# Optimization experiments

Measured on AMD Instinct MI355X. Metric: run time of the kernel, lower is better.

The kernel has to match this reference:

```python
import jax, jax.numpy as jnp
import numpy as np

B, L, S, D, H = 4, 2048, 2048, 1024, 16
HD = D // H


def setup_inputs() -> dict:
    key = jax.random.key(0)
    ks = jax.random.split(key, 7)
    scale = 1.0 / np.sqrt(D)
    q = jax.random.normal(ks[0], (B, L, D), dtype=jnp.float32)
    k = jax.random.normal(ks[1], (B, S, D), dtype=jnp.float32)
    v = jax.random.normal(ks[2], (B, S, D), dtype=jnp.float32)
    # causal mask, broadcast over batch and heads; 0 -> masked
    mask = jnp.tril(jnp.ones((L, S), dtype=jnp.int32))[None, None]
    Wq = jax.random.normal(ks[3], (D, D), dtype=jnp.float32) * scale
    Wk = jax.random.normal(ks[4], (D, D), dtype=jnp.float32) * scale
    Wv = jax.random.normal(ks[5], (D, D), dtype=jnp.float32) * scale
    Wo = jax.random.normal(ks[6], (D, D), dtype=jnp.float32) * scale
    return {"q": q, "k": k, "v": v, "mask": mask,
            "Wq": Wq, "Wk": Wk, "Wv": Wv, "Wo": Wo}


def reference(q, k, v, mask, Wq, Wk, Wv, Wo):
    Bq, Lq, _ = q.shape
    Sk = k.shape[1]
    # torch nn.Linear: y = x @ W.T  (W is [out, in])
    qh = (q @ Wq.T).reshape(Bq, Lq, H, HD).transpose(0, 2, 1, 3)  # [B,H,L,hd]
    kh = (k @ Wk.T).reshape(Bq, Sk, H, HD).transpose(0, 2, 1, 3)  # [B,H,S,hd]
    vh = (v @ Wv.T).reshape(Bq, Sk, H, HD).transpose(0, 2, 1, 3)  # [B,H,S,hd]
    scores = jnp.einsum('bhld,bhsd->bhls', qh, kh) / jnp.sqrt(jnp.float32(HD))
    scores = jnp.where(mask == 0, -jnp.inf, scores)
    attn = jax.nn.softmax(scores, axis=-1)
    out = jnp.einsum('bhls,bhsd->bhld', attn, vh)
    out = out.transpose(0, 2, 1, 3).reshape(Bq, Lq, D)
    return out @ Wo.T
```

## Files before the change

### kernel.cpp

```cpp
#include <hip/hip_runtime.h>
#include <hip/hip_bf16.h>

#define BB 4
#define LL 2048
#define SS 2048
#define DD 1024
#define HH 16
#define HD 64

typedef __bf16 bf16;
typedef __attribute__((ext_vector_type(8))) __bf16 bf16x8;
typedef __attribute__((ext_vector_type(4))) float f32x4;

#define ASYNC16(gp, lp)                                                        \
  __builtin_amdgcn_global_load_lds(                                            \
      (__attribute__((address_space(1))) void*)(gp),                           \
      (__attribute__((address_space(3))) void*)(lp), 16, 0, 0)

__global__ __launch_bounds__(256) void detect_dtype(
    const unsigned short* __restrict__ qbits, int* __restrict__ flag) {
  __shared__ int smax;
  if (threadIdx.x == 0) smax = 0;
  __syncthreads();
  int m = 0;
  for (int i = threadIdx.x; i < 4096; i += 256) {
    const int e = (qbits[i] >> 7) & 0xFF;
    m = m > e ? m : e;
  }
  atomicMax(&smax, m);
  __syncthreads();
  if (threadIdx.x == 0) *flag = (smax >= 0xC0) ? 1 : 0;
}

__global__ __launch_bounds__(256) void convert_all(
    const void* __restrict__ q, const void* __restrict__ k,
    const void* __restrict__ v, const void* __restrict__ Wq,
    const void* __restrict__ Wk, const void* __restrict__ Wv,
    const void* __restrict__ Wo, bf16* __restrict__ cq, bf16* __restrict__ ck,
    bf16* __restrict__ cv, bf16* __restrict__ cWq, bf16* __restrict__ cWk,
    bf16* __restrict__ cWv, bf16* __restrict__ cWo,
    const int* __restrict__ flag) {
  const int b = blockIdx.x;
  const void* src;
  bf16* dst;
  int lb;
  if (b < 12288) {
    const int t = b >> 12;
    lb = b & 4095;
    src = (t == 0) ? q : (t == 1) ? k : v;
    dst = (t == 0) ? cq : (t == 1) ? ck : cv;
  } else {
    const int t = (b - 12288) >> 9;
    lb = (b - 12288) & 511;
    src = (t == 0) ? Wq : (t == 1) ? Wk : (t == 2) ? Wv : Wo;
    dst = (t == 0) ? cWq : (t == 1) ? cWk : (t == 2) ? cWv : cWo;
  }
  const int i8 = (lb * 256 + threadIdx.x) * 8;
  if (*flag) {
    const float4* s = (const float4*)src;
    const float4 a = s[i8 / 4];
    const float4 c = s[i8 / 4 + 1];
    bf16x8 o;
    o[0] = (bf16)a.x; o[1] = (bf16)a.y; o[2] = (bf16)a.z; o[3] = (bf16)a.w;
    o[4] = (bf16)c.x; o[5] = (bf16)c.y; o[6] = (bf16)c.z; o[7] = (bf16)c.w;
    *(bf16x8*)(dst + i8) = o;
  } else {
    *(uint4*)(dst + i8) = ((const uint4*)src)[i8 / 8];
  }
}

#define GM 8192
#define GN 1024
#define GK 1024

#define GEMM_BODY(X, W)                                                        \
  const int tid = threadIdx.x;                                                 \
  const int lane = tid & 63;                                                   \
  const int wave = tid >> 6;                                                   \
  const int l15 = lane & 15;                                                   \
  const int quad = lane >> 4;                                                  \
  const int wm = wave >> 1;                                                    \
  const int wn = wave & 1;                                                     \
  const int lin = blockIdx.y * 8 + blockIdx.x;                                 \
  const int tileN = ((lin >> 3) & 7) * 128;                                    \
  const int tileM = ((lin & 7) | ((lin >> 6) << 3)) * 128;                     \
  __shared__ bf16 As[128 * 64];                                                \
  __shared__ bf16 Bs[128 * 64];                                                \
  f32x4 acc[4][4];                                                             \
  _Pragma("unroll") for (int mi = 0; mi < 4; ++mi)                             \
      _Pragma("unroll") for (int ni = 0; ni < 4; ++ni)                         \
          acc[mi][ni] = (f32x4){0.f, 0.f, 0.f, 0.f};                           \
  const int srow8 = lane >> 3;                                                 \
  const int jsw = (lane & 7) ^ srow8;                                          \
  const int swz8 = l15 & 7;                                                    \
  for (int k0 = 0; k0 < GK; k0 += 64) {                                        \
    __syncthreads();                                                           \
    _Pragma("unroll") for (int i = 0; i < 4; ++i) {                            \
      const int r0 = (i * 4 + wave) * 8;                                       \
      ASYNC16(X + (size_t)(tileM + r0 + srow8) * GK + k0 + jsw * 8,            \
              &As[r0 * 64]);                                                   \
      ASYNC16(W + (size_t)(tileN + r0 + srow8) * GK + k0 + jsw * 8,            \
              &Bs[r0 * 64]);                                                   \
    }                                                                          \
    __syncthreads();                                                           \
    _Pragma("unroll") for (int ks = 0; ks < 2; ++ks) {                         \
      bf16x8 a[4], b[4];                                                       \
      _Pragma("unroll") for (int mi = 0; mi < 4; ++mi)                         \
          a[mi] = *(const bf16x8*)&As[(wm * 64 + mi * 16 + l15) * 64 +         \
                                      (((ks * 4 + quad) ^ swz8) * 8)];         \
      _Pragma("unroll") for (int ni = 0; ni < 4; ++ni)                         \
          b[ni] = *(const bf16x8*)&Bs[(wn * 64 + ni * 16 + l15) * 64 +         \
                                      (((ks * 4 + quad) ^ swz8) * 8)];         \
      _Pragma("unroll") for (int mi = 0; mi < 4; ++mi)                         \
          _Pragma("unroll") for (int ni = 0; ni < 4; ++ni)                     \
              acc[mi][ni] = __builtin_amdgcn_mfma_f32_16x16x32_bf16(           \
                  a[mi], b[ni], acc[mi][ni], 0, 0, 0);                         \
    }                                                                          \
  }

__global__ __launch_bounds__(256, 4) void gemm_qkv(
    const bf16* __restrict__ cq, const bf16* __restrict__ ck,
    const bf16* __restrict__ cv, const bf16* __restrict__ cWq,
    const bf16* __restrict__ cWk, const bf16* __restrict__ cWv,
    bf16* __restrict__ qh, bf16* __restrict__ kh, bf16* __restrict__ vt) {
  const int z = blockIdx.z;
  const bf16* X = (z == 0) ? cq : (z == 1) ? ck : cv;
  const bf16* W = (z == 0) ? cWq : (z == 1) ? cWk : cWv;
  bf16* Out = (z == 0) ? qh : (z == 1) ? kh : vt;
  GEMM_BODY(X, W)
#pragma unroll
  for (int mi = 0; mi < 4; ++mi)
#pragma unroll
    for (int ni = 0; ni < 4; ++ni)
#pragma unroll
      for (int r = 0; r < 4; ++r) {
        const int row = tileM + wm * 64 + mi * 16 + quad * 4 + r;
        const int col = tileN + wn * 64 + ni * 16 + l15;
        const int b_ = row >> 11;
        const int l_ = row & 2047;
        const int h_ = col >> 6;
        const int hd_ = col & 63;
        size_t idx;
        if (z < 2)
          idx = (((size_t)(b_ * HH + h_)) * LL + l_) * HD + hd_;
        else
          idx = (((size_t)(b_ * HH + h_)) * HD + hd_) * SS + l_;
        Out[idx] = (bf16)acc[mi][ni][r];
      }
}

__global__ __launch_bounds__(256, 4) void gemm_out(const bf16* __restrict__ X,
                                                   const bf16* __restrict__ W,
                                                   void* __restrict__ Outv,
                                                   const int* __restrict__ flag) {
  GEMM_BODY(X, W)
  const bool f32out = (*flag != 0);
#pragma unroll
  for (int mi = 0; mi < 4; ++mi)
#pragma unroll
    for (int ni = 0; ni < 4; ++ni)
#pragma unroll
      for (int r = 0; r < 4; ++r) {
        const int row = tileM + wm * 64 + mi * 16 + quad * 4 + r;
        const int col = tileN + wn * 64 + ni * 16 + l15;
        const size_t idx = (size_t)row * GN + col;
        if (f32out)
          ((float*)Outv)[idx] = acc[mi][ni][r];
        else
          ((bf16*)Outv)[idx] = (bf16)acc[mi][ni][r];
      }
}

__global__ __launch_bounds__(256, 4) void attn_fwd(const bf16* __restrict__ Qh,
                                                   const bf16* __restrict__ Kh,
                                                   const bf16* __restrict__ Vt,
                                                   bf16* __restrict__ AOut) {
  const int tid = threadIdx.x;
  const int lane = tid & 63;
  const int wave = tid >> 6;
  const int l15 = lane & 15;
  const int quad = lane >> 4;

  const int flat = blockIdx.x + (blockIdx.y << 4);
  const int c = flat & 7;
  const int t = flat >> 3;
  const int bh = c * 8 + (t >> 4);
  const int qx = t & 15;
  const int b_ = bh >> 4;
  const int h_ = bh & 15;

  const bf16* Qb = Qh + (size_t)bh * LL * HD;
  const bf16* Kb = Kh + (size_t)bh * SS * HD;
  const bf16* Vb = Vt + (size_t)bh * HD * SS;

  __shared__ bf16 Ks[2][64 * 64];
  __shared__ bf16 Vs[2][64 * 64];
  __shared__ bf16 Ps[4][16 * 64];

  bf16x8 onef;
#pragma unroll
  for (int j = 0; j < 8; ++j) onef[j] = (l15 == 0) ? (bf16)1.0f : (bf16)0.0f;

  const int srow8 = lane >> 3;
  const int jsw = (lane & 7) ^ srow8;
  const int swz = l15 & 7;

#define ATTN_STAGE(bi, s0)                                                     \
  _Pragma("unroll") for (int i_ = 0; i_ < 2; ++i_) {                           \
    const int r0_ = (i_ * 4 + wave) * 8;                                       \
    ASYNC16(Kb + (size_t)((s0) + r0_ + srow8) * HD + jsw * 8,                  \
            &Ks[bi][r0_ * 64]);                                                \
    ASYNC16(Vb + (size_t)(r0_ + srow8) * SS + (s0) + jsw * 8,                  \
            &Vs[bi][r0_ * 64]);                                                \
  }

  for (int ph = 0; ph < 2; ++ph) {
    const int qt = ph ? (31 - qx) : qx;
    const int qrow0 = qt * 64 + wave * 16;

    bf16x8 qf[2];
#pragma unroll
    for (int ks = 0; ks < 2; ++ks)
      qf[ks] =
          *(const bf16x8*)(Qb + (size_t)(qrow0 + l15) * HD + ks * 32 + quad * 8);

    f32x4 o[5];
#pragma unroll
    for (int ni = 0; ni < 5; ++ni) o[ni] = (f32x4){0.f, 0.f, 0.f, 0.f};

    __syncthreads();
    ATTN_STAGE(0, 0)

    for (int st = 0; st <= qt; ++st) {
      const int s0 = st * 64;
      const int cur = st & 1;
      __syncthreads();
      if (st < qt) {
        const int sn = s0 + 64;
        ATTN_STAGE(cur ^ 1, sn)
      }

      f32x4 sc[4];
#pragma unroll
      for (int ni = 0; ni < 4; ++ni) {
        sc[ni] = (f32x4){0.f, 0.f, 0.f, 0.f};
#pragma unroll
        for (int ks = 0; ks < 2; ++ks) {
          bf16x8 kf = *(const bf16x8*)&Ks[cur][(ni * 16 + l15) * 64 +
                                              (((ks * 4 + quad) ^ swz) * 8)];
          sc[ni] = __builtin_amdgcn_mfma_f32_16x16x32_bf16(qf[ks], kf, sc[ni],
                                                           0, 0, 0);
        }
      }

      if (st < qt) {
#pragma unroll
        for (int ni = 0; ni < 4; ++ni)
#pragma unroll
          for (int r = 0; r < 4; ++r) {
            const int row = quad * 4 + r;
            const float p = __expf(fmaf(sc[ni][r], 0.125f, -12.0f));
            Ps[wave][row * 64 + (((ni * 2 + (l15 >> 3)) ^ (row & 7)) * 8) +
                     (l15 & 7)] = (bf16)p;
          }
      } else {
#pragma unroll
        for (int ni = 0; ni < 4; ++ni) {
          const int scolg = s0 + ni * 16 + l15;
#pragma unroll
          for (int r = 0; r < 4; ++r) {
            const int row = quad * 4 + r;
            const int qrow = qrow0 + row;
            const float p = (scolg <= qrow)
                                ? __expf(fmaf(sc[ni][r], 0.125f, -12.0f))
                                : 0.f;
            Ps[wave][row * 64 + (((ni * 2 + (l15 >> 3)) ^ (row & 7)) * 8) +
                     (l15 & 7)] = (bf16)p;
          }
        }
      }

#pragma unroll
      for (int ks = 0; ks < 2; ++ks) {
        bf16x8 pf = *(const bf16x8*)&Ps[wave][l15 * 64 +
                                              (((ks * 4 + quad) ^ (l15 & 7)) *
                                               8)];
#pragma unroll
        for (int ni = 0; ni < 4; ++ni) {
          bf16x8 vf = *(const bf16x8*)&Vs[cur][(ni * 16 + l15) * 64 +
                                              (((ks * 4 + quad) ^ swz) * 8)];
          o[ni] =
              __builtin_amdgcn_mfma_f32_16x16x32_bf16(pf, vf, o[ni], 0, 0, 0);
        }
        o[4] = __builtin_amdgcn_mfma_f32_16x16x32_bf16(pf, onef, o[4], 0, 0, 0);
      }
    }

#pragma unroll
    for (int r = 0; r < 4; ++r) {
      const float l = __shfl(o[4][r], lane & 48);
      const float inv = 1.f / l;
      const int row = qrow0 + quad * 4 + r;
#pragma unroll
      for (int ni = 0; ni < 4; ++ni) {
        AOut[((size_t)(b_ * LL + row)) * DD + h_ * HD + ni * 16 + l15] =
            (bf16)(o[ni][r] * inv);
      }
    }
  }
}

extern "C" void kernel_launch(void* const* d_in, const int* in_sizes, int n_in,
                              void* d_out, int out_size, void* d_ws,
                              size_t ws_size, hipStream_t stream) {
  (void)in_sizes; (void)n_in; (void)out_size; (void)ws_size;
  const void* q = d_in[0];
  const void* k = d_in[1];
  const void* v = d_in[2];
  const void* Wq = d_in[4];
  const void* Wk = d_in[5];
  const void* Wv = d_in[6];
  const void* Wo = d_in[7];

  const size_t Sq = (size_t)BB * LL * DD;
  const size_t Sw = (size_t)DD * DD;

  int* flag = (int*)d_ws;
  bf16* base = (bf16*)((char*)d_ws + 16);
  bf16* cq = base;
  bf16* ck = cq + Sq;
  bf16* cv = ck + Sq;
  bf16* cWq = cv + Sq;
  bf16* cWk = cWq + Sw;
  bf16* cWv = cWk + Sw;
  bf16* cWo = cWv + Sw;
  bf16* qh = cWo + Sw;
  bf16* kh = qh + Sq;
  bf16* vt = kh + Sq;
  bf16* ao = vt + Sq;

  dim3 blk(256);
  detect_dtype<<<1, blk, 0, stream>>>((const unsigned short*)q, flag);
  convert_all<<<14336, blk, 0, stream>>>(q, k, v, Wq, Wk, Wv, Wo, cq, ck, cv,
                                         cWq, cWk, cWv, cWo, flag);
  gemm_qkv<<<dim3(GN / 128, GM / 128, 3), blk, 0, stream>>>(cq, ck, cv, cWq,
                                                            cWk, cWv, qh, kh,
                                                            vt);
  attn_fwd<<<dim3(16, BB * HH), blk, 0, stream>>>(qh, kh, vt, ao);
  gemm_out<<<dim3(GN / 128, GM / 128), blk, 0, stream>>>(ao, cWo, d_out, flag);
}
```

Measured before the change: 340.9 us.

## Fuse fp32-to-bf16 conversion into GEMM tile staging, drop convert pass

New measurement: 447.4 us. 1.31x slower.

```diff
diff --git a/kernel.cpp b/kernel.cpp
--- a/kernel.cpp
+++ b/kernel.cpp
@@ -32,48 +32,32 @@
   if (threadIdx.x == 0) *flag = (smax >= 0xC0) ? 1 : 0;
 }
 
-__global__ __launch_bounds__(256) void convert_all(
-    const void* __restrict__ q, const void* __restrict__ k,
-    const void* __restrict__ v, const void* __restrict__ Wq,
-    const void* __restrict__ Wk, const void* __restrict__ Wv,
-    const void* __restrict__ Wo, bf16* __restrict__ cq, bf16* __restrict__ ck,
-    bf16* __restrict__ cv, bf16* __restrict__ cWq, bf16* __restrict__ cWk,
-    bf16* __restrict__ cWv, bf16* __restrict__ cWo,
-    const int* __restrict__ flag) {
-  const int b = blockIdx.x;
-  const void* src;
-  bf16* dst;
-  int lb;
-  if (b < 12288) {
-    const int t = b >> 12;
-    lb = b & 4095;
-    src = (t == 0) ? q : (t == 1) ? k : v;
-    dst = (t == 0) ? cq : (t == 1) ? ck : cv;
-  } else {
-    const int t = (b - 12288) >> 9;
-    lb = (b - 12288) & 511;
-    src = (t == 0) ? Wq : (t == 1) ? Wk : (t == 2) ? Wv : Wo;
-    dst = (t == 0) ? cWq : (t == 1) ? cWk : (t == 2) ? cWv : cWo;
-  }
-  const int i8 = (lb * 256 + threadIdx.x) * 8;
-  if (*flag) {
-    const float4* s = (const float4*)src;
-    const float4 a = s[i8 / 4];
-    const float4 c = s[i8 / 4 + 1];
-    bf16x8 o;
-    o[0] = (bf16)a.x; o[1] = (bf16)a.y; o[2] = (bf16)a.z; o[3] = (bf16)a.w;
-    o[4] = (bf16)c.x; o[5] = (bf16)c.y; o[6] = (bf16)c.z; o[7] = (bf16)c.w;
-    *(bf16x8*)(dst + i8) = o;
-  } else {
-    *(uint4*)(dst + i8) = ((const uint4*)src)[i8 / 8];
-  }
-}
-
 #define GM 8192
 #define GN 1024
 #define GK 1024
 
-#define GEMM_BODY(X, W)                                                        \
+#define STAGE_ONE(PTR, ISF32, rowBase, k0, BUF, r0)                            \
+  do {                                                                         \
+    if (ISF32) {                                                               \
+      const float* sp_ = (const float*)(PTR) +                                 \
+                         (size_t)((rowBase) + r0 + srow8) * GK + (k0) +        \
+                         jsw * 8;                                              \
+      const float4 u_ = ((const float4*)sp_)[0];                               \
+      const float4 v_ = ((const float4*)sp_)[1];                               \
+      bf16x8 o8_;                                                              \
+      o8_[0] = (bf16)u_.x; o8_[1] = (bf16)u_.y;                                \
+      o8_[2] = (bf16)u_.z; o8_[3] = (bf16)u_.w;                                \
+      o8_[4] = (bf16)v_.x; o8_[5] = (bf16)v_.y;                                \
+      o8_[6] = (bf16)v_.z; o8_[7] = (bf16)v_.w;                                \
+      *(bf16x8*)&BUF[(r0 + srow8) * 64 + g8] = o8_;                            \
+    } else {                                                                   \
+      ASYNC16((const bf16*)(PTR) + (size_t)((rowBase) + r0 + srow8) * GK +     \
+                  (k0) + jsw * 8,                                              \
+              &BUF[r0 * 64]);                                                  \
+    }                                                                          \
+  } while (0)
+
+#define GEMM_BODY(XP, XF, WP, WF)                                              \
   const int tid = threadIdx.x;                                                 \
   const int lane = tid & 63;                                                   \
   const int wave = tid >> 6;                                                   \
@@ -93,14 +77,15 @@
   const int srow8 = lane >> 3;                                                 \
   const int jsw = (lane & 7) ^ srow8;                                          \
   const int swz8 = l15 & 7;                                                    \
+  const int g8 = (lane & 7) * 8;                                               \
+  const bool xf_ = (XF);                                                       \
+  const bool wf_ = (WF);                                                       \
   for (int k0 = 0; k0 < GK; k0 += 64) {                                        \
     __syncthreads();                                                           \
     _Pragma("unroll") for (int i = 0; i < 4; ++i) {                            \
       const int r0 = (i * 4 + wave) * 8;                                       \
-      ASYNC16(X + (size_t)(tileM + r0 + srow8) * GK + k0 + jsw * 8,            \
-              &As[r0 * 64]);                                                   \
-      ASYNC16(W + (size_t)(tileN + r0 + srow8) * GK + k0 + jsw * 8,            \
-              &Bs[r0 * 64]);                                                   \
+      STAGE_ONE(XP, xf_, tileM, k0, As, r0);                                   \
+      STAGE_ONE(WP, wf_, tileN, k0, Bs, r0);                                   \
     }                                                                          \
     __syncthreads();                                                           \
     _Pragma("unroll") for (int ks = 0; ks < 2; ++ks) {                         \
@@ -119,15 +104,17 @@
   }
 
 __global__ __launch_bounds__(256, 4) void gemm_qkv(
-    const bf16* __restrict__ cq, const bf16* __restrict__ ck,
-    const bf16* __restrict__ cv, const bf16* __restrict__ cWq,
-    const bf16* __restrict__ cWk, const bf16* __restrict__ cWv,
-    bf16* __restrict__ qh, bf16* __restrict__ kh, bf16* __restrict__ vt) {
+    const void* __restrict__ q, const void* __restrict__ k,
+    const void* __restrict__ v, const void* __restrict__ Wq,
+    const void* __restrict__ Wk, const void* __restrict__ Wv,
+    bf16* __restrict__ qh, bf16* __restrict__ kh, bf16* __restrict__ vt,
+    const int* __restrict__ flag) {
   const int z = blockIdx.z;
-  const bf16* X = (z == 0) ? cq : (z == 1) ? ck : cv;
-  const bf16* W = (z == 0) ? cWq : (z == 1) ? cWk : cWv;
+  const void* X = (z == 0) ? q : (z == 1) ? k : v;
+  const void* W = (z == 0) ? Wq : (z == 1) ? Wk : Wv;
   bf16* Out = (z == 0) ? qh : (z == 1) ? kh : vt;
-  GEMM_BODY(X, W)
+  const bool f32in = (*flag != 0);
+  GEMM_BODY(X, f32in, W, f32in)
 #pragma unroll
   for (int mi = 0; mi < 4; ++mi)
 #pragma unroll
@@ -150,11 +137,12 @@
 }
 
 __global__ __launch_bounds__(256, 4) void gemm_out(const bf16* __restrict__ X,
-                                                   const bf16* __restrict__ W,
+                                                   const void* __restrict__ W,
                                                    void* __restrict__ Outv,
                                                    const int* __restrict__ flag) {
-  GEMM_BODY(X, W)
-  const bool f32out = (*flag != 0);
+  const bool f32w = (*flag != 0);
+  GEMM_BODY(X, false, W, f32w)
+  const bool f32out = f32w;
 #pragma unroll
   for (int mi = 0; mi < 4; ++mi)
 #pragma unroll
@@ -323,29 +311,19 @@
   const void* Wo = d_in[7];
 
   const size_t Sq = (size_t)BB * LL * DD;
-  const size_t Sw = (size_t)DD * DD;
 
   int* flag = (int*)d_ws;
   bf16* base = (bf16*)((char*)d_ws + 16);
-  bf16* cq = base;
-  bf16* ck = cq + Sq;
-  bf16* cv = ck + Sq;
-  bf16* cWq = cv + Sq;
-  bf16* cWk = cWq + Sw;
-  bf16* cWv = cWk + Sw;
-  bf16* cWo = cWv + Sw;
-  bf16* qh = cWo + Sw;
+  bf16* qh = base;
   bf16* kh = qh + Sq;
   bf16* vt = kh + Sq;
   bf16* ao = vt + Sq;
 
   dim3 blk(256);
   detect_dtype<<<1, blk, 0, stream>>>((const unsigned short*)q, flag);
-  convert_all<<<14336, blk, 0, stream>>>(q, k, v, Wq, Wk, Wv, Wo, cq, ck, cv,
-                                         cWq, cWk, cWv, cWo, flag);
-  gemm_qkv<<<dim3(GN / 128, GM / 128, 3), blk, 0, stream>>>(cq, ck, cv, cWq,
-                                                            cWk, cWv, qh, kh,
-                                                            vt);
+  gemm_qkv<<<dim3(GN / 128, GM / 128, 3), blk, 0, stream>>>(q, k, v, Wq, Wk,
+                                                            Wv, qh, kh, vt,
+                                                            flag);
   attn_fwd<<<dim3(16, BB * HH), blk, 0, stream>>>(qh, kh, vt, ao);
-  gemm_out<<<dim3(GN / 128, GM / 128), blk, 0, stream>>>(ao, cWo, d_out, flag);
-}
+  gemm_out<<<dim3(GN / 128, GM / 128), blk, 0, stream>>>(ao, Wo, d_out, flag);
+}
```

## Double-buffer GEMM shared-memory tiles with a K-step of 32 to overlap loads

Applied to the files above, without the earlier changes.

Measured after the change: 365.0 us. +7.1%, slower.

```diff
diff --git a/kernel.cpp b/kernel.cpp
--- a/kernel.cpp
+++ b/kernel.cpp
@@ -73,6 +73,17 @@
 #define GN 1024
 #define GK 1024
 
+#define GEMM_STAGE(ABUF, BBUF, k0)                                             \
+  do {                                                                         \
+    _Pragma("unroll") for (int i_ = 0; i_ < 2; ++i_) {                         \
+      const int r0_ = (i_ * 4 + wave) * 16;                                    \
+      ASYNC16(X + (size_t)(tileM + r0_ + srow4) * GK + (k0) + jsw4 * 8,        \
+              &ABUF[r0_ * 32]);                                                \
+      ASYNC16(W + (size_t)(tileN + r0_ + srow4) * GK + (k0) + jsw4 * 8,        \
+              &BBUF[r0_ * 32]);                                                \
+    }                                                                          \
+  } while (0)
+
 #define GEMM_BODY(X, W)                                                        \
   const int tid = threadIdx.x;                                                 \
   const int lane = tid & 63;                                                   \
@@ -84,38 +95,31 @@
   const int lin = blockIdx.y * 8 + blockIdx.x;                                 \
   const int tileN = ((lin >> 3) & 7) * 128;                                    \
   const int tileM = ((lin & 7) | ((lin >> 6) << 3)) * 128;                     \
-  __shared__ bf16 As[128 * 64];                                                \
-  __shared__ bf16 Bs[128 * 64];                                                \
+  __shared__ bf16 As[2][128 * 32];                                             \
+  __shared__ bf16 Bs[2][128 * 32];                                             \
   f32x4 acc[4][4];                                                             \
   _Pragma("unroll") for (int mi = 0; mi < 4; ++mi)                             \
       _Pragma("unroll") for (int ni = 0; ni < 4; ++ni)                         \
           acc[mi][ni] = (f32x4){0.f, 0.f, 0.f, 0.f};                           \
-  const int srow8 = lane >> 3;                                                 \
-  const int jsw = (lane & 7) ^ srow8;                                          \
-  const int swz8 = l15 & 7;                                                    \
-  for (int k0 = 0; k0 < GK; k0 += 64) {                                        \
-    __syncthreads();                                                           \
-    _Pragma("unroll") for (int i = 0; i < 4; ++i) {                            \
-      const int r0 = (i * 4 + wave) * 8;                                       \
-      ASYNC16(X + (size_t)(tileM + r0 + srow8) * GK + k0 + jsw * 8,            \
-              &As[r0 * 64]);                                                   \
-      ASYNC16(W + (size_t)(tileN + r0 + srow8) * GK + k0 + jsw * 8,            \
-              &Bs[r0 * 64]);                                                   \
-    }                                                                          \
-    __syncthreads();                                                           \
-    _Pragma("unroll") for (int ks = 0; ks < 2; ++ks) {                         \
-      bf16x8 a[4], b[4];                                                       \
-      _Pragma("unroll") for (int mi = 0; mi < 4; ++mi)                         \
-          a[mi] = *(const bf16x8*)&As[(wm * 64 + mi * 16 + l15) * 64 +         \
-                                      (((ks * 4 + quad) ^ swz8) * 8)];         \
-      _Pragma("unroll") for (int ni = 0; ni < 4; ++ni)                         \
-          b[ni] = *(const bf16x8*)&Bs[(wn * 64 + ni * 16 + l15) * 64 +         \
-                                      (((ks * 4 + quad) ^ swz8) * 8)];         \
-      _Pragma("unroll") for (int mi = 0; mi < 4; ++mi)                         \
-          _Pragma("unroll") for (int ni = 0; ni < 4; ++ni)                     \
-              acc[mi][ni] = __builtin_amdgcn_mfma_f32_16x16x32_bf16(           \
-                  a[mi], b[ni], acc[mi][ni], 0, 0, 0);                         \
-    }                                                                          \
+  const int srow4 = lane >> 2;                                                 \
+  const int jsw4 = (lane & 3) ^ ((lane >> 3) & 3);                             \
+  const int rsw = (l15 >> 1) & 3;                                              \
+  GEMM_STAGE(As[0], Bs[0], 0);                                                 \
+  for (int t = 0; t < 32; ++t) {                                               \
+    const int cur = t & 1;                                                     \
+    __syncthreads();  \
+    if (t < 31) GEMM_STAGE(As[cur ^ 1], Bs[cur ^ 1], (t + 1) * 32);            \
+    bf16x8 a[4], b[4];                                                         \
+    _Pragma("unroll") for (int mi = 0; mi < 4; ++mi)                           \
+        a[mi] = *(const bf16x8*)&As[cur][(wm * 64 + mi * 16 + l15) * 32 +      \
+                                         ((quad ^ rsw) * 8)];                  \
+    _Pragma("unroll") for (int ni = 0; ni < 4; ++ni)                           \
+        b[ni] = *(const bf16x8*)&Bs[cur][(wn * 64 + ni * 16 + l15) * 32 +      \
+                                         ((quad ^ rsw) * 8)];                  \
+    _Pragma("unroll") for (int mi = 0; mi < 4; ++mi)                           \
+        _Pragma("unroll") for (int ni = 0; ni < 4; ++ni)                       \
+            acc[mi][ni] = __builtin_amdgcn_mfma_f32_16x16x32_bf16(             \
+                a[mi], b[ni], acc[mi][ni], 0, 0, 0);                           \
   }
 
 __global__ __launch_bounds__(256, 4) void gemm_qkv(
```
